# Performance work log

Measured on AMD Instinct MI355X. Metric: run time of the kernel, lower is better.

Reference implementation:

```python
import jax, jax.numpy as jnp
import numpy as np

DIM = 512
HEADS = 8
HD = DIM // HEADS          # 64
WIN = 64
HALF = WIN // 2            # 32 -> each query sees [i-32, i+32], 65 keys


def setup_inputs() -> dict:
    key = jax.random.key(0)
    k0, k1, k2 = jax.random.split(key, 3)
    x = jax.random.normal(k0, (4, 4096, DIM), dtype=jnp.float32)
    W_qkv = jax.random.normal(k1, (DIM, 3 * DIM), dtype=jnp.float32) * 0.02
    b_qkv = jnp.zeros((3 * DIM,), dtype=jnp.float32)
    W_proj = jax.random.normal(k2, (DIM, DIM), dtype=jnp.float32) * 0.02
    b_proj = jnp.zeros((DIM,), dtype=jnp.float32)
    return {"x": x, "W_qkv": W_qkv, "b_qkv": b_qkv, "W_proj": W_proj, "b_proj": b_proj}


def _sliding_window_attn(q, k, v):
    # q,k,v: [B, H, S, Dh]. Banded attention: query i attends keys [i-HALF, i+HALF].
    B, H, S, Dh = q.shape
    scale = Dh ** -0.5
    pos = jnp.arange(S)
    offsets = list(range(-HALF, HALF + 1))  # fixed small set (65)
    # Banded scores via diagonal shifts -> [B, H, S, 2*HALF+1]; never materialize [S,S].
    scores = []
    for o in offsets:
        k_sh = jnp.roll(k, -o, axis=2)                       # key at position i+o
        s = jnp.einsum('bhsd,bhsd->bhs', q, k_sh) * scale
        valid = (pos + o >= 0) & (pos + o < S)
        s = jnp.where(valid[None, None, :], s, -jnp.inf)
        scores.append(s)
    scores = jnp.stack(scores, axis=-1)                      # [B,H,S,65]
    p = jax.nn.softmax(scores, axis=-1)
    out = jnp.zeros_like(q)
    for idx, o in enumerate(offsets):
        out = out + p[..., idx:idx + 1] * jnp.roll(v, -o, axis=2)
    return out


def reference(x, W_qkv, b_qkv, W_proj, b_proj):
    B, S, _ = x.shape
    qkv = (x @ W_qkv + b_qkv).reshape(B, S, 3, HEADS, HD)
    qkv = jnp.transpose(qkv, (2, 0, 3, 1, 4))                # [3, B, H, S, Dh]
    q, k, v = qkv[0], qkv[1], qkv[2]
    attn = _sliding_window_attn(q, k, v)                     # [B, H, S, Dh]
    attn = jnp.transpose(attn, (0, 2, 1, 3)).reshape(B, S, DIM)
    # dropout is identity in eval mode
    return attn @ W_proj + b_proj
```

## Files before the change

### kernel.cpp

```cpp
#include <hip/hip_runtime.h>

#define DIMc 512
#define Sc   4096
#define Bc   4
#define Mc   (Bc*Sc)
#define N1c  (3*DIMc)
#define Kc   DIMc
#define HDc  64
#define HALFW 32

using short8  = __attribute__((ext_vector_type(8))) short;
using ushort4v= __attribute__((ext_vector_type(4))) unsigned short;
using f32x4   = __attribute__((ext_vector_type(4))) float;

__device__ __forceinline__ unsigned short f2b(float f) {
  unsigned int u = __builtin_bit_cast(unsigned int, f);
  u += 0x7FFFu + ((u >> 16) & 1u);
  return (unsigned short)(u >> 16);
}

__device__ __forceinline__ void gll16(const unsigned short* g, char* lds_uniform) {
  __builtin_amdgcn_global_load_lds(
      (const __attribute__((address_space(1))) unsigned int*)g,
      (__attribute__((address_space(3))) unsigned int*)lds_uniform,
      16, 0, 0);
}

__global__ void k_convert_x(const float* __restrict__ x, unsigned short* __restrict__ xb) {
  int t = blockIdx.x * 256 + threadIdx.x;
  int row = t >> 6;
  int s   = t & 63;
  const float* src = x + (size_t)row * DIMc + s * 8;
  float4 a = *(const float4*)(src);
  float4 b = *(const float4*)(src + 4);
  int sp = (s & ~7) | ((s & 7) ^ (row & 7));
  short8 v;
  v[0]=(short)f2b(a.x); v[1]=(short)f2b(a.y); v[2]=(short)f2b(a.z); v[3]=(short)f2b(a.w);
  v[4]=(short)f2b(b.x); v[5]=(short)f2b(b.y); v[6]=(short)f2b(b.z); v[7]=(short)f2b(b.w);
  *(short8*)(xb + (size_t)row * DIMc + sp * 8) = v;
}

__global__ void k_convert_wT(const float* __restrict__ W, unsigned short* __restrict__ wT, int Nn) {
  int t = blockIdx.x * 256 + threadIdx.x;
  int s = t / Nn;
  int n = t - s * Nn;
  short8 v;
#pragma unroll
  for (int j = 0; j < 8; ++j) v[j] = (short)f2b(W[(size_t)(s * 8 + j) * Nn + n]);
  int sp = (s & ~7) | ((s & 7) ^ (n & 7));
  *(short8*)(wT + (size_t)n * Kc + sp * 8) = v;
}

__device__ __forceinline__ void gemm_main2(const unsigned short* __restrict__ A,
                                           const unsigned short* __restrict__ Bt,
                                           int m0, int n0, int lane, int w,
                                           char* smem, f32x4 acc[4][4]) {
  int g = lane >> 4;
  int mbase = (w & 1) * 64;
  int nbase = (w >> 1) * 64;
  const int NKT = Kc / 64;

  auto STAGE = [&](int buf, int kt) {
    char* base = smem + (buf << 15);
#pragma unroll
    for (int i = 0; i < 4; ++i) {
      int cbase = i * 256 + w * 64;
      int c = cbase + lane;
      int row = c >> 3, sl = c & 7;
      gll16(A + (size_t)(m0 + row) * Kc + kt * 64 + sl * 8, base + cbase * 16);
    }
#pragma unroll
    for (int i = 0; i < 4; ++i) {
      int cbase = i * 256 + w * 64;
      int c = cbase + lane;
      int row = c >> 3, sl = c & 7;
      gll16(Bt + (size_t)(n0 + row) * Kc + kt * 64 + sl * 8, base + 16384 + cbase * 16);
    }
  };

  STAGE(0, 0);
  int cur = 0;
  for (int kt = 0; kt < NKT; ++kt) {
    if (kt + 1 < NKT) {
      STAGE(cur ^ 1, kt + 1);
      asm volatile("s_waitcnt vmcnt(8)" ::: "memory");
    } else {
      asm volatile("s_waitcnt vmcnt(0)" ::: "memory");
    }
    __builtin_amdgcn_s_barrier();
    __builtin_amdgcn_sched_barrier(0);
    unsigned short* As = (unsigned short*)(smem + (cur << 15));
    unsigned short* Bs = (unsigned short*)(smem + (cur << 15) + 16384);
#pragma unroll
    for (int ksub = 0; ksub < 2; ++ksub) {
      short8 af[4], bf[4];
#pragma unroll
      for (int mt = 0; mt < 4; ++mt) {
        int row = mbase + mt * 16 + (lane & 15);
        int slot = ((ksub << 2) + g) ^ (row & 7);
        af[mt] = *(const short8*)(As + row * 64 + slot * 8);
      }
#pragma unroll
      for (int ct = 0; ct < 4; ++ct) {
        int row = nbase + ct * 16 + (lane & 15);
        int slot = ((ksub << 2) + g) ^ (row & 7);
        bf[ct] = *(const short8*)(Bs + row * 64 + slot * 8);
      }
#pragma unroll
      for (int mt = 0; mt < 4; ++mt)
#pragma unroll
        for (int ct = 0; ct < 4; ++ct)
          acc[mt][ct] = __builtin_amdgcn_mfma_f32_16x16x32_bf16(af[mt], bf[ct], acc[mt][ct], 0, 0, 0);
    }
    __builtin_amdgcn_sched_barrier(0);
    __builtin_amdgcn_s_barrier();
    cur ^= 1;
  }
}

__global__ void k_gemm_qkv(const unsigned short* __restrict__ xb,
                           const unsigned short* __restrict__ wT,
                           const float* __restrict__ bias,
                           unsigned short* __restrict__ qb,
                           unsigned short* __restrict__ kb,
                           unsigned short* __restrict__ vb) {
  __shared__ __align__(16) char smem[65536];
  int bid = blockIdx.x;
  int x = bid & 7, i = bid >> 3;
  int bm = x * 16 + i / 12;
  int bn = i - (i / 12) * 12;
  int m0 = bm * 128, n0 = bn * 128;
  int lane = threadIdx.x & 63, w = threadIdx.x >> 6, g = lane >> 4, nl = lane & 15;
  f32x4 acc[4][4];
#pragma unroll
  for (int i2 = 0; i2 < 4; ++i2)
#pragma unroll
    for (int j = 0; j < 4; ++j) acc[i2][j] = f32x4{0.f, 0.f, 0.f, 0.f};
  gemm_main2(xb, wT, m0, n0, lane, w, smem, acc);

  unsigned short* Ct = (unsigned short*)smem;
  float bsv[4];
#pragma unroll
  for (int ct = 0; ct < 4; ++ct) bsv[ct] = bias[n0 + (w >> 1) * 64 + ct * 16 + nl];
  bool isV = (n0 >= 1024);
  if (!isV) {
#pragma unroll
    for (int mt = 0; mt < 4; ++mt)
#pragma unroll
      for (int ct = 0; ct < 4; ++ct)
#pragma unroll
        for (int r = 0; r < 4; ++r) {
          int m = (w & 1) * 64 + mt * 16 + 4 * g + r;
          int n = (w >> 1) * 64 + ct * 16 + nl;
          Ct[m * 128 + (n ^ (g << 4))] = f2b(acc[mt][ct][r] + bsv[ct]);
        }
  } else {
#pragma unroll
    for (int mt = 0; mt < 4; ++mt)
#pragma unroll
      for (int ct = 0; ct < 4; ++ct) {
        int n = (w >> 1) * 64 + ct * 16 + nl;
        int mchunk = (w & 1) * 16 + mt * 4 + g;
        ushort4v pk;
#pragma unroll
        for (int r = 0; r < 4; ++r) pk[r] = f2b(acc[mt][ct][r] + bsv[ct]);
        *(ushort4v*)(Ct + n * 128 + ((mchunk ^ (n & 15)) << 2)) = pk;
      }
  }
  __syncthreads();
  int tid = threadIdx.x;
  if (!isV) {
    int tt = n0 >> 9;
    unsigned short* dst0 = tt ? kb : qb;
#pragma unroll
    for (int i2 = 0; i2 < 8; ++i2) {
      int cid = i2 * 256 + tid;
      int row = cid >> 4, c = cid & 15;
      int gg = (row >> 2) & 3;
      short8 vv = *(const short8*)(Ct + row * 128 + ((c ^ (gg << 1)) << 3));
      int m = m0 + row, b = m >> 12, s = m & 4095;
      int ng = n0 + c * 8, h = (ng >> 6) & 7, d0 = ng & 63;
      *(short8*)(dst0 + ((size_t)(b * 8 + h) * Sc + s) * HDc + d0) = vv;
    }
  } else {
#pragma unroll
    for (int i2 = 0; i2 < 8; ++i2) {
      int cid = i2 * 256 + tid;
      int n = cid & 127, m8i = cid >> 7;
      int cpair = (m8i * 2) ^ (n & 14);
      short8 vv = *(const short8*)(Ct + n * 128 + (cpair << 2));
      if (n & 1) vv = __builtin_shufflevector(vv, vv, 4, 5, 6, 7, 0, 1, 2, 3);
      int ng = n0 + n, h = (ng >> 6) & 7, d = ng & 63;
      int m = m0 + m8i * 8, b = m >> 12, s = m & 4095;
      *(short8*)(vb + ((size_t)(b * 8 + h) * HDc + d) * Sc + s) = vv;
    }
  }
}

__global__ void k_attn(const unsigned short* __restrict__ qb,
                       const unsigned short* __restrict__ kb,
                       const unsigned short* __restrict__ vb,
                       unsigned short* __restrict__ attnb) {
  __shared__ __align__(16) char smem[40960];
  unsigned short* Qt = (unsigned short*)smem;
  unsigned short* Kt = (unsigned short*)(smem + 8192);
  unsigned short* Vt = (unsigned short*)(smem + 24576);
  unsigned short* Pt = (unsigned short*)smem;
  int bid = blockIdx.x;
  int x = bid & 7, i = bid >> 3;
  int bh = x * 4 + (i >> 6), qt = i & 63;
  int q0 = qt * 64;
  int tid = threadIdx.x;
  int lane = tid & 63, w = tid >> 6, g = lane >> 4;

  const unsigned short* qsrc = qb + ((long)bh * Sc + q0) * HDc;
#pragma unroll
  for (int i2 = 0; i2 < 2; ++i2) {
    int wc = i2 * 4 + w;
    int cid = wc * 64 + lane, row = cid >> 3, sl = cid & 7;
    gll16(qsrc + row * 64 + (sl ^ (row & 7)) * 8, (char*)Qt + wc * 1024);
  }
  const unsigned short* ksrc = kb + ((long)bh * Sc + q0 - HALFW) * HDc;
#pragma unroll
  for (int i2 = 0; i2 < 4; ++i2) {
    int wc = i2 * 4 + w;
    int cid = wc * 64 + lane, row = cid >> 3, sl = cid & 7;
    gll16(ksrc + row * 64 + (sl ^ (row & 7)) * 8, (char*)Kt + wc * 1024);
  }
  const unsigned short* vsrc = vb + (long)bh * HDc * Sc + (q0 - HALFW);
#pragma unroll
  for (int i2 = 0; i2 < 4; ++i2) {
    int wc = i2 * 4 + w;
    int cid = wc * 64 + lane, row = cid >> 4, sl = cid & 15;
    gll16(vsrc + (long)row * Sc + (sl ^ (row & 15)) * 8, (char*)Vt + wc * 1024);
  }
  __syncthreads();

  f32x4 sc[8];
#pragma unroll
  for (int ct = 0; ct < 8; ++ct) sc[ct] = f32x4{0.f, 0.f, 0.f, 0.f};
#pragma unroll
  for (int ksub = 0; ksub < 2; ++ksub) {
    int arow = w * 16 + (lane & 15);
    int aslot = ((ksub << 2) + g) ^ (arow & 7);
    short8 af = *(const short8*)(Qt + arow * 64 + aslot * 8);
#pragma unroll
    for (int ct = 0; ct < 8; ++ct) {
      int brow = ct * 16 + (lane & 15);
      int bslot = ((ksub << 2) + g) ^ (brow & 7);
      short8 bf = *(const short8*)(Kt + brow * 64 + bslot * 8);
      sc[ct] = __builtin_amdgcn_mfma_f32_16x16x32_bf16(af, bf, sc[ct], 0, 0, 0);
    }
  }
  float rsum[4] = {0.f, 0.f, 0.f, 0.f};
#pragma unroll
  for (int ct = 0; ct < 8; ++ct) {
    int keyl = ct * 16 + (lane & 15);
    int keyg = q0 - HALFW + keyl;
#pragma unroll
    for (int r = 0; r < 4; ++r) {
      int q = q0 + w * 16 + 4 * g + r;
      int dlt = keyg - q;
      bool valid = (dlt >= -HALFW) && (dlt <= HALFW) && (keyg >= 0) && (keyg < Sc);
      float pv = valid ? __expf(sc[ct][r] * 0.125f) : 0.f;
      sc[ct][r] = pv;
      rsum[r] += pv;
    }
  }
#pragma unroll
  for (int r = 0; r < 4; ++r) {
    float v = rsum[r];
    v += __shfl_xor(v, 1); v += __shfl_xor(v, 2); v += __shfl_xor(v, 4); v += __shfl_xor(v, 8);
    rsum[r] = 1.0f / v;
  }
  __syncthreads();
#pragma unroll
  for (int ct = 0; ct < 8; ++ct) {
    int keyl = ct * 16 + (lane & 15);
#pragma unroll
    for (int r = 0; r < 4; ++r) {
      int prow = w * 16 + 4 * g + r;
      int sp = (keyl >> 3) ^ (prow & 15);
      Pt[prow * 128 + sp * 8 + (keyl & 7)] = f2b(sc[ct][r]);
    }
  }
  __syncthreads();
  f32x4 o[4];
#pragma unroll
  for (int i2 = 0; i2 < 4; ++i2) o[i2] = f32x4{0.f, 0.f, 0.f, 0.f};
#pragma unroll
  for (int ks = 0; ks < 4; ++ks) {
    int arow = w * 16 + (lane & 15);
    int aslot = ((ks << 2) + g) ^ (arow & 15);
    short8 af = *(const short8*)(Pt + arow * 128 + aslot * 8);
#pragma unroll
    for (int ct2 = 0; ct2 < 4; ++ct2) {
      int vrow = ct2 * 16 + (lane & 15);
      int vslot = ((ks << 2) + g) ^ (vrow & 15);
      short8 bf = *(const short8*)(Vt + vrow * 128 + vslot * 8);
      o[ct2] = __builtin_amdgcn_mfma_f32_16x16x32_bf16(af, bf, o[ct2], 0, 0, 0);
    }
  }
  int h = bh & 7, b = bh >> 3;
#pragma unroll
  for (int ct2 = 0; ct2 < 4; ++ct2) {
    int d = ct2 * 16 + (lane & 15);
    int col = h * 64 + d;
    int slot = col >> 3;
#pragma unroll
    for (int r = 0; r < 4; ++r) {
      int q = q0 + w * 16 + 4 * g + r;
      int sp = (slot & ~7) | ((slot & 7) ^ (q & 7));
      attnb[((size_t)b * Sc + q) * DIMc + sp * 8 + (col & 7)] = f2b(o[ct2][r] * rsum[r]);
    }
  }
}

__global__ void k_gemm_proj(const unsigned short* __restrict__ ab,
                            const unsigned short* __restrict__ wT,
                            const float* __restrict__ bias,
                            float* __restrict__ out) {
  __shared__ __align__(16) char smem[65536];
  int bid = blockIdx.x;
  int x = bid & 7, i = bid >> 3;
  int bm = x * 16 + (i >> 2), bn = i & 3;
  int m0 = bm * 128, n0 = bn * 128;
  int lane = threadIdx.x & 63, w = threadIdx.x >> 6, g = lane >> 4;
  f32x4 acc[4][4];
#pragma unroll
  for (int i2 = 0; i2 < 4; ++i2)
#pragma unroll
    for (int j = 0; j < 4; ++j) acc[i2][j] = f32x4{0.f, 0.f, 0.f, 0.f};
  gemm_main2(ab, wT, m0, n0, lane, w, smem, acc);
#pragma unroll
  for (int ct = 0; ct < 4; ++ct) {
    int n = n0 + (w >> 1) * 64 + ct * 16 + (lane & 15);
    float bs = bias[n];
#pragma unroll
    for (int mt = 0; mt < 4; ++mt) {
#pragma unroll
      for (int r = 0; r < 4; ++r) {
        int m = m0 + (w & 1) * 64 + mt * 16 + 4 * g + r;
        out[(size_t)m * DIMc + n] = acc[mt][ct][r] + bs;
      }
    }
  }
}

extern "C" void kernel_launch(void* const* d_in, const int* in_sizes, int n_in,
                              void* d_out, int out_size, void* d_ws, size_t ws_size,
                              hipStream_t stream) {
  const float* x     = (const float*)d_in[0];
  const float* Wqkv  = (const float*)d_in[1];
  const float* bqkv  = (const float*)d_in[2];
  const float* Wproj = (const float*)d_in[3];
  const float* bproj = (const float*)d_in[4];
  float* out = (float*)d_out;

  char* ws = (char*)d_ws;
  const size_t SZ_QKV = (size_t)32 * Sc * HDc * 2;
  const size_t SZ_ATT = (size_t)Mc * DIMc * 2;
  size_t off = 0;
  unsigned short* qb    = (unsigned short*)(ws + off); off += SZ_QKV;
  unsigned short* kb    = (unsigned short*)(ws + off); off += SZ_QKV;
  unsigned short* vb    = (unsigned short*)(ws + off); off += SZ_QKV;
  unsigned short* attnb = (unsigned short*)(ws + off); off += SZ_ATT;
  unsigned short* xb    = (unsigned short*)(ws + off); off += SZ_ATT;
  unsigned short* wqkvT = (unsigned short*)(ws + off); off += (size_t)N1c * Kc * 2;
  unsigned short* wprjT = (unsigned short*)(ws + off); off += (size_t)DIMc * Kc * 2;
  if (ws_size < off) return;

  k_convert_x <<<dim3(4096), dim3(256), 0, stream>>>(x, xb);
  k_convert_wT<<<dim3(384),  dim3(256), 0, stream>>>(Wqkv, wqkvT, N1c);
  k_convert_wT<<<dim3(128),  dim3(256), 0, stream>>>(Wproj, wprjT, DIMc);
  k_gemm_qkv  <<<dim3(1536), dim3(256), 0, stream>>>(xb, wqkvT, bqkv, qb, kb, vb);
  k_attn      <<<dim3(2048), dim3(256), 0, stream>>>(qb, kb, vb, attnb);
  k_gemm_proj <<<dim3(512),  dim3(256), 0, stream>>>(attnb, wprjT, bproj, out);
}
```

Before: 81.94 us.

## Enlarge QKV GEMM tile to 256x256 with 512 threads and split-phase LDS pipeline

Rewrites the QKV projection GEMM to compute 256x256 output tiles per block with 8 waves and 128KB of dynamic LDS. K-slices are staged asynchronously in half-tiles, interleaved with MFMA phases and guarded by barriers and setprio. The aim is higher operand reuse per LDS byte and better overlap of global loads with compute. In exchange the grid shrinks to 384 blocks, which fill the CUs unevenly, and occupancy drops to one block per CU. The launch also depends on more than 64KB of dynamic LDS being allowed.

```diff
diff --git a/kernel.cpp b/kernel.cpp
--- a/kernel.cpp
+++ b/kernel.cpp
@@ -118,77 +118,173 @@
   }
 }
 
-__global__ void k_gemm_qkv(const unsigned short* __restrict__ xb,
-                           const unsigned short* __restrict__ wT,
-                           const float* __restrict__ bias,
-                           unsigned short* __restrict__ qb,
-                           unsigned short* __restrict__ kb,
-                           unsigned short* __restrict__ vb) {
-  __shared__ __align__(16) char smem[65536];
+__global__ __launch_bounds__(512, 2) void k_gemm_qkv(
+    const unsigned short* __restrict__ xb, const unsigned short* __restrict__ wT,
+    const float* __restrict__ bias, unsigned short* __restrict__ qb,
+    unsigned short* __restrict__ kb, unsigned short* __restrict__ vb) {
+  extern __shared__ __align__(16) char smem[];
   int bid = blockIdx.x;
-  int x = bid & 7, i = bid >> 3;
-  int bm = x * 16 + i / 12;
-  int bn = i - (i / 12) * 12;
-  int m0 = bm * 128, n0 = bn * 128;
-  int lane = threadIdx.x & 63, w = threadIdx.x >> 6, g = lane >> 4, nl = lane & 15;
-  f32x4 acc[4][4];
-#pragma unroll
-  for (int i2 = 0; i2 < 4; ++i2)
-#pragma unroll
-    for (int j = 0; j < 4; ++j) acc[i2][j] = f32x4{0.f, 0.f, 0.f, 0.f};
-  gemm_main2(xb, wT, m0, n0, lane, w, smem, acc);
-
+  int xcd = bid & 7, ii = bid >> 3;
+  int bm = xcd * 8 + ii / 6;
+  int bn = ii - (ii / 6) * 6;
+  int m0 = bm * 256, n0 = bn * 256;
+  int tid = threadIdx.x;
+  int lane = tid & 63, w = tid >> 6;
+  int g = lane >> 4, nl = lane & 15;
+  int wr = w >> 2, wc = w & 3;
+
+  f32x4 acc[8][4];
+#pragma unroll
+  for (int i = 0; i < 8; ++i)
+#pragma unroll
+    for (int j = 0; j < 4; ++j) acc[i][j] = f32x4{0.f, 0.f, 0.f, 0.f};
+
+  auto STG = [&](int which, int q, int h, int kt) {
+    const unsigned short* src = which ? (wT + (size_t)(n0 + h * 128) * Kc)
+                                      : (xb + (size_t)(m0 + h * 128) * Kc);
+    src += kt * 64;
+    char* dst = smem + (which ? 65536 : 0) + (q << 15) + h * 16384;
+#pragma unroll
+    for (int i2 = 0; i2 < 2; ++i2) {
+      int cid = (w * 2 + i2) * 64 + lane;
+      int row = cid >> 3, sl = cid & 7;
+      gll16(src + (size_t)row * Kc + sl * 8, dst + (w * 2 + i2) * 1024);
+    }
+  };
+
+  STG(0, 0, 0, 0); STG(1, 0, 0, 0); STG(0, 0, 1, 0); STG(1, 0, 1, 0);
+  STG(0, 1, 0, 1); STG(1, 1, 0, 1);
+  asm volatile("s_waitcnt vmcnt(4)" ::: "memory");
+  __builtin_amdgcn_s_barrier();
+
+  for (int kt = 0; kt < 8; ++kt) {
+    int q = kt & 1;
+    unsigned short* As = (unsigned short*)(smem + (q << 15));
+    unsigned short* Bs = (unsigned short*)(smem + 65536 + (q << 15));
+#pragma unroll
+    for (int mh = 0; mh < 2; ++mh) {
+      short8 af[4][2];
+#pragma unroll
+      for (int mt2 = 0; mt2 < 4; ++mt2)
+#pragma unroll
+        for (int ks = 0; ks < 2; ++ks) {
+          int row = wr * 128 + (mh * 4 + mt2) * 16 + nl;
+          int slot = ((ks << 2) + g) ^ (row & 7);
+          af[mt2][ks] = *(const short8*)(As + row * 64 + slot * 8);
+        }
+      {
+        short8 bf[2][2];
+#pragma unroll
+        for (int ct2 = 0; ct2 < 2; ++ct2)
+#pragma unroll
+          for (int ks = 0; ks < 2; ++ks) {
+            int row = wc * 64 + ct2 * 16 + nl;
+            int slot = ((ks << 2) + g) ^ (row & 7);
+            bf[ct2][ks] = *(const short8*)(Bs + row * 64 + slot * 8);
+          }
+        if (mh == 0) { if (kt + 1 < 8) STG(0, (kt + 1) & 1, 1, kt + 1); }
+        else         { if (kt + 2 < 8) STG(0, q, 0, kt + 2); }
+        __builtin_amdgcn_s_barrier();
+        asm volatile("s_waitcnt lgkmcnt(0)" ::: "memory");
+        __builtin_amdgcn_sched_barrier(0);
+        __builtin_amdgcn_s_setprio(1);
+#pragma unroll
+        for (int mt2 = 0; mt2 < 4; ++mt2)
+#pragma unroll
+          for (int ct2 = 0; ct2 < 2; ++ct2)
+#pragma unroll
+            for (int ks = 0; ks < 2; ++ks)
+              acc[mh * 4 + mt2][ct2] = __builtin_amdgcn_mfma_f32_16x16x32_bf16(
+                  af[mt2][ks], bf[ct2][ks], acc[mh * 4 + mt2][ct2], 0, 0, 0);
+        __builtin_amdgcn_s_setprio(0);
+        __builtin_amdgcn_sched_barrier(0);
+        __builtin_amdgcn_s_barrier();
+      }
+      {
+        short8 bf[2][2];
+#pragma unroll
+        for (int ct2 = 0; ct2 < 2; ++ct2)
+#pragma unroll
+          for (int ks = 0; ks < 2; ++ks) {
+            int row = wc * 64 + (2 + ct2) * 16 + nl;
+            int slot = ((ks << 2) + g) ^ (row & 7);
+            bf[ct2][ks] = *(const short8*)(Bs + row * 64 + slot * 8);
+          }
+        if (mh == 0) { if (kt + 1 < 8) STG(1, (kt + 1) & 1, 1, kt + 1); }
+        else         { if (kt + 2 < 8) STG(1, q, 0, kt + 2); }
+        __builtin_amdgcn_s_barrier();
+        asm volatile("s_waitcnt lgkmcnt(0)" ::: "memory");
+        __builtin_amdgcn_sched_barrier(0);
+        __builtin_amdgcn_s_setprio(1);
+#pragma unroll
+        for (int mt2 = 0; mt2 < 4; ++mt2)
+#pragma unroll
+          for (int ct2 = 0; ct2 < 2; ++ct2)
+#pragma unroll
+            for (int ks = 0; ks < 2; ++ks)
+              acc[mh * 4 + mt2][2 + ct2] = __builtin_amdgcn_mfma_f32_16x16x32_bf16(
+                  af[mt2][ks], bf[ct2][ks], acc[mh * 4 + mt2][2 + ct2], 0, 0, 0);
+        __builtin_amdgcn_s_setprio(0);
+        __builtin_amdgcn_sched_barrier(0);
+        if (mh == 1) {
+          if (kt < 6)       { asm volatile("s_waitcnt vmcnt(4)" ::: "memory"); }
+          else if (kt == 6) { asm volatile("s_waitcnt vmcnt(0)" ::: "memory"); }
+        }
+        __builtin_amdgcn_s_barrier();
+      }
+    }
+  }
+  __syncthreads();
+
+  float bsv[4];
+#pragma unroll
+  for (int ct = 0; ct < 4; ++ct) bsv[ct] = bias[n0 + wc * 64 + ct * 16 + nl];
   unsigned short* Ct = (unsigned short*)smem;
-  float bsv[4];
-#pragma unroll
-  for (int ct = 0; ct < 4; ++ct) bsv[ct] = bias[n0 + (w >> 1) * 64 + ct * 16 + nl];
   bool isV = (n0 >= 1024);
   if (!isV) {
 #pragma unroll
-    for (int mt = 0; mt < 4; ++mt)
+    for (int mt = 0; mt < 8; ++mt)
 #pragma unroll
       for (int ct = 0; ct < 4; ++ct)
 #pragma unroll
         for (int r = 0; r < 4; ++r) {
-          int m = (w & 1) * 64 + mt * 16 + 4 * g + r;
-          int n = (w >> 1) * 64 + ct * 16 + nl;
-          Ct[m * 128 + (n ^ (g << 4))] = f2b(acc[mt][ct][r] + bsv[ct]);
+          int m = wr * 128 + mt * 16 + 4 * g + r;
+          int n = wc * 64 + ct * 16 + nl;
+          Ct[m * 256 + (n ^ (g << 4))] = f2b(acc[mt][ct][r] + bsv[ct]);
         }
   } else {
 #pragma unroll
-    for (int mt = 0; mt < 4; ++mt)
+    for (int mt = 0; mt < 8; ++mt)
 #pragma unroll
       for (int ct = 0; ct < 4; ++ct) {
-        int n = (w >> 1) * 64 + ct * 16 + nl;
-        int mchunk = (w & 1) * 16 + mt * 4 + g;
+        int n = wc * 64 + ct * 16 + nl;
+        int mch = wr * 32 + mt * 4 + g;
         ushort4v pk;
 #pragma unroll
         for (int r = 0; r < 4; ++r) pk[r] = f2b(acc[mt][ct][r] + bsv[ct]);
-        *(ushort4v*)(Ct + n * 128 + ((mchunk ^ (n & 15)) << 2)) = pk;
+        *(ushort4v*)(Ct + n * 256 + ((mch ^ (n & 15)) << 2)) = pk;
       }
   }
   __syncthreads();
-  int tid = threadIdx.x;
   if (!isV) {
-    int tt = n0 >> 9;
-    unsigned short* dst0 = tt ? kb : qb;
-#pragma unroll
-    for (int i2 = 0; i2 < 8; ++i2) {
-      int cid = i2 * 256 + tid;
-      int row = cid >> 4, c = cid & 15;
+    unsigned short* dst0 = (n0 >= 512) ? kb : qb;
+#pragma unroll
+    for (int it = 0; it < 16; ++it) {
+      int cid = it * 512 + tid;
+      int row = cid >> 5, c = cid & 31;
       int gg = (row >> 2) & 3;
-      short8 vv = *(const short8*)(Ct + row * 128 + ((c ^ (gg << 1)) << 3));
+      short8 vv = *(const short8*)(Ct + row * 256 + ((c ^ (gg << 1)) << 3));
       int m = m0 + row, b = m >> 12, s = m & 4095;
       int ng = n0 + c * 8, h = (ng >> 6) & 7, d0 = ng & 63;
       *(short8*)(dst0 + ((size_t)(b * 8 + h) * Sc + s) * HDc + d0) = vv;
     }
   } else {
 #pragma unroll
-    for (int i2 = 0; i2 < 8; ++i2) {
-      int cid = i2 * 256 + tid;
-      int n = cid & 127, m8i = cid >> 7;
+    for (int it = 0; it < 16; ++it) {
+      int cid = it * 512 + tid;
+      int n = cid >> 5, m8i = cid & 31;
       int cpair = (m8i * 2) ^ (n & 14);
-      short8 vv = *(const short8*)(Ct + n * 128 + (cpair << 2));
+      short8 vv = *(const short8*)(Ct + n * 256 + (cpair << 2));
       if (n & 1) vv = __builtin_shufflevector(vv, vv, 4, 5, 6, 7, 0, 1, 2, 3);
       int ng = n0 + n, h = (ng >> 6) & 7, d = ng & 63;
       int m = m0 + m8i * 8, b = m >> 12, s = m & 4095;
@@ -373,7 +469,7 @@
   k_convert_x <<<dim3(4096), dim3(256), 0, stream>>>(x, xb);
   k_convert_wT<<<dim3(384),  dim3(256), 0, stream>>>(Wqkv, wqkvT, N1c);
   k_convert_wT<<<dim3(128),  dim3(256), 0, stream>>>(Wproj, wprjT, DIMc);
-  k_gemm_qkv  <<<dim3(1536), dim3(256), 0, stream>>>(xb, wqkvT, bqkv, qb, kb, vb);
+  k_gemm_qkv  <<<dim3(384),  dim3(512), 131072, stream>>>(xb, wqkvT, bqkv, qb, kb, vb);
   k_attn      <<<dim3(2048), dim3(256), 0, stream>>>(qb, kb, vb, attnb);
   k_gemm_proj <<<dim3(512),  dim3(256), 0, stream>>>(attnb, wprjT, bproj, out);
 }
```

Result: slower. 86.24 us (+5.3%).

## Fuse fp32-to-bf16 conversion of x into QKV GEMM A-tile loads

Applied to the files above, without the earlier changes.

The QKV GEMM now reads fp32 x directly, converting to bf16 in registers and writing swizzled tiles into LDS, so the separate x-conversion kernel and its bf16 intermediate buffer go away. The two weight-conversion launches are merged into one kernel. This removes a full write and read of the bf16 copy of x plus launch overhead. In exchange, the GEMM reads twice as many A bytes (fp32), and each A tile is converted 12 times, once per N-block, instead of once. It also uses a register-staged A load with vmcnt(0) waits that may reduce overlap.

```diff
diff --git a/kernel.cpp b/kernel.cpp
--- a/kernel.cpp
+++ b/kernel.cpp
@@ -26,22 +26,12 @@
       16, 0, 0);
 }
 
-__global__ void k_convert_x(const float* __restrict__ x, unsigned short* __restrict__ xb) {
-  int t = blockIdx.x * 256 + threadIdx.x;
-  int row = t >> 6;
-  int s   = t & 63;
-  const float* src = x + (size_t)row * DIMc + s * 8;
-  float4 a = *(const float4*)(src);
-  float4 b = *(const float4*)(src + 4);
-  int sp = (s & ~7) | ((s & 7) ^ (row & 7));
-  short8 v;
-  v[0]=(short)f2b(a.x); v[1]=(short)f2b(a.y); v[2]=(short)f2b(a.z); v[3]=(short)f2b(a.w);
-  v[4]=(short)f2b(b.x); v[5]=(short)f2b(b.y); v[6]=(short)f2b(b.z); v[7]=(short)f2b(b.w);
-  *(short8*)(xb + (size_t)row * DIMc + sp * 8) = v;
-}
-
-__global__ void k_convert_wT(const float* __restrict__ W, unsigned short* __restrict__ wT, int Nn) {
-  int t = blockIdx.x * 256 + threadIdx.x;
+__global__ void k_convert_w2(const float* __restrict__ W1, unsigned short* __restrict__ wT1,
+                             const float* __restrict__ W2, unsigned short* __restrict__ wT2) {
+  int b = blockIdx.x;
+  const float* W; unsigned short* wT; int Nn, t;
+  if (b < 384) { W = W1; wT = wT1; Nn = N1c;  t = b * 256 + threadIdx.x; }
+  else         { W = W2; wT = wT2; Nn = DIMc; t = (b - 384) * 256 + threadIdx.x; }
   int s = t / Nn;
   int n = t - s * Nn;
   short8 v;
@@ -118,25 +108,100 @@
   }
 }
 
-__global__ void k_gemm_qkv(const unsigned short* __restrict__ xb,
-                           const unsigned short* __restrict__ wT,
-                           const float* __restrict__ bias,
-                           unsigned short* __restrict__ qb,
-                           unsigned short* __restrict__ kb,
-                           unsigned short* __restrict__ vb) {
+__global__ __launch_bounds__(256, 2) void k_gemm_qkv(
+    const float* __restrict__ x, const unsigned short* __restrict__ wT,
+    const float* __restrict__ bias, unsigned short* __restrict__ qb,
+    unsigned short* __restrict__ kb, unsigned short* __restrict__ vb) {
   __shared__ __align__(16) char smem[65536];
   int bid = blockIdx.x;
-  int x = bid & 7, i = bid >> 3;
-  int bm = x * 16 + i / 12;
-  int bn = i - (i / 12) * 12;
+  int xcd = bid & 7, ii = bid >> 3;
+  int bm = xcd * 16 + ii / 12;
+  int bn = ii - (ii / 12) * 12;
   int m0 = bm * 128, n0 = bn * 128;
-  int lane = threadIdx.x & 63, w = threadIdx.x >> 6, g = lane >> 4, nl = lane & 15;
+  int tid = threadIdx.x;
+  int lane = tid & 63, w = tid >> 6, g = lane >> 4, nl = lane & 15;
+
   f32x4 acc[4][4];
 #pragma unroll
   for (int i2 = 0; i2 < 4; ++i2)
 #pragma unroll
     for (int j = 0; j < 4; ++j) acc[i2][j] = f32x4{0.f, 0.f, 0.f, 0.f};
-  gemm_main2(xb, wT, m0, n0, lane, w, smem, acc);
+
+  float4 fa[4][2];
+  auto LOAD_A = [&](int kt) {
+#pragma unroll
+    for (int i = 0; i < 4; ++i) {
+      int gid = i * 256 + tid;
+      int row = gid >> 3, sl = gid & 7;
+      const float* src = x + (size_t)(m0 + row) * DIMc + kt * 64 + sl * 8;
+      fa[i][0] = *(const float4*)src;
+      fa[i][1] = *(const float4*)(src + 4);
+    }
+  };
+  auto WRITE_A = [&](int buf) {
+    unsigned short* As = (unsigned short*)(smem + (buf << 15));
+#pragma unroll
+    for (int i = 0; i < 4; ++i) {
+      int gid = i * 256 + tid;
+      int row = gid >> 3, sl = gid & 7;
+      short8 v;
+      v[0]=(short)f2b(fa[i][0].x); v[1]=(short)f2b(fa[i][0].y);
+      v[2]=(short)f2b(fa[i][0].z); v[3]=(short)f2b(fa[i][0].w);
+      v[4]=(short)f2b(fa[i][1].x); v[5]=(short)f2b(fa[i][1].y);
+      v[6]=(short)f2b(fa[i][1].z); v[7]=(short)f2b(fa[i][1].w);
+      *(short8*)(As + row * 64 + (sl ^ (row & 7)) * 8) = v;
+    }
+  };
+  auto STAGE_B = [&](int buf, int kt) {
+    char* base = smem + (buf << 15) + 16384;
+#pragma unroll
+    for (int i = 0; i < 4; ++i) {
+      int cbase = i * 256 + w * 64;
+      int c = cbase + lane;
+      int row = c >> 3, sl = c & 7;
+      gll16(wT + (size_t)(n0 + row) * Kc + kt * 64 + sl * 8, base + cbase * 16);
+    }
+  };
+
+  LOAD_A(0);
+  STAGE_B(0, 0);
+  asm volatile("s_waitcnt vmcnt(0)" ::: "memory");
+  WRITE_A(0);
+  __syncthreads();
+
+  int mbase = (w & 1) * 64, nbase = (w >> 1) * 64;
+  for (int kt = 0; kt < 8; ++kt) {
+    int cur = kt & 1;
+    if (kt + 1 < 8) { LOAD_A(kt + 1); STAGE_B(cur ^ 1, kt + 1); }
+    unsigned short* As = (unsigned short*)(smem + (cur << 15));
+    unsigned short* Bs = (unsigned short*)(smem + (cur << 15) + 16384);
+#pragma unroll
+    for (int ksub = 0; ksub < 2; ++ksub) {
+      short8 af[4], bf[4];
+#pragma unroll
+      for (int mt = 0; mt < 4; ++mt) {
+        int row = mbase + mt * 16 + nl;
+        int slot = ((ksub << 2) + g) ^ (row & 7);
+        af[mt] = *(const short8*)(As + row * 64 + slot * 8);
+      }
+#pragma unroll
+      for (int ct = 0; ct < 4; ++ct) {
+        int row = nbase + ct * 16 + nl;
+        int slot = ((ksub << 2) + g) ^ (row & 7);
+        bf[ct] = *(const short8*)(Bs + row * 64 + slot * 8);
+      }
+#pragma unroll
+      for (int mt = 0; mt < 4; ++mt)
+#pragma unroll
+        for (int ct = 0; ct < 4; ++ct)
+          acc[mt][ct] = __builtin_amdgcn_mfma_f32_16x16x32_bf16(af[mt], bf[ct], acc[mt][ct], 0, 0, 0);
+    }
+    if (kt + 1 < 8) {
+      asm volatile("s_waitcnt vmcnt(0)" ::: "memory");
+      WRITE_A(cur ^ 1);
+    }
+    __syncthreads();
+  }
 
   unsigned short* Ct = (unsigned short*)smem;
   float bsv[4];
@@ -168,10 +233,8 @@
       }
   }
   __syncthreads();
-  int tid = threadIdx.x;
   if (!isV) {
-    int tt = n0 >> 9;
-    unsigned short* dst0 = tt ? kb : qb;
+    unsigned short* dst0 = (n0 >= 512) ? kb : qb;
 #pragma unroll
     for (int i2 = 0; i2 < 8; ++i2) {
       int cid = i2 * 256 + tid;
@@ -365,15 +428,12 @@
   unsigned short* kb    = (unsigned short*)(ws + off); off += SZ_QKV;
   unsigned short* vb    = (unsigned short*)(ws + off); off += SZ_QKV;
   unsigned short* attnb = (unsigned short*)(ws + off); off += SZ_ATT;
-  unsigned short* xb    = (unsigned short*)(ws + off); off += SZ_ATT;
   unsigned short* wqkvT = (unsigned short*)(ws + off); off += (size_t)N1c * Kc * 2;
   unsigned short* wprjT = (unsigned short*)(ws + off); off += (size_t)DIMc * Kc * 2;
   if (ws_size < off) return;
 
-  k_convert_x <<<dim3(4096), dim3(256), 0, stream>>>(x, xb);
-  k_convert_wT<<<dim3(384),  dim3(256), 0, stream>>>(Wqkv, wqkvT, N1c);
-  k_convert_wT<<<dim3(128),  dim3(256), 0, stream>>>(Wproj, wprjT, DIMc);
-  k_gemm_qkv  <<<dim3(1536), dim3(256), 0, stream>>>(xb, wqkvT, bqkv, qb, kb, vb);
+  k_convert_w2<<<dim3(512),  dim3(256), 0, stream>>>(Wqkv, wqkvT, Wproj, wprjT);
+  k_gemm_qkv  <<<dim3(1536), dim3(256), 0, stream>>>(x, wqkvT, bqkv, qb, kb, vb);
   k_attn      <<<dim3(2048), dim3(256), 0, stream>>>(qb, kb, vb, attnb);
   k_gemm_proj <<<dim3(512),  dim3(256), 0, stream>>>(attnb, wprjT, bproj, out);
 }
```

After: 89.85 us. 1.1x slower.
